# Kernel tuning notes

Hardware: AMD Instinct MI355X
Metric: run time of the kernel (lower is better)

## Reference

```python
import jax, jax.numpy as jnp
import numpy as np

B, S, D = 2, 2048, 2048
NH, NKV = 16, 4
HD = D // NH          # 128
Q_DIM = NH * HD       # 2048
KV_DIM = NKV * HD     # 512
N_REP = NH // NKV     # 4


def setup_inputs() -> dict:
    key = jax.random.key(0)
    k1, k2, k3, k4 = jax.random.split(key, 4)
    x = jax.random.normal(k1, (B, S, D), dtype=jnp.float32)
    freqs_cis = jax.random.normal(k2, (S, HD), dtype=jnp.float32)
    Wqkv = jax.random.normal(k3, (Q_DIM + 2 * KV_DIM, D), dtype=jnp.float32) * (D ** -0.5)
    Wo = jax.random.normal(k4, (D, Q_DIM), dtype=jnp.float32) * (Q_DIM ** -0.5)
    return {"x": x, "freqs_cis": freqs_cis, "Wqkv": Wqkv, "Wo": Wo}


def _apply_rope(xq, xk, freqs_cis):
    # xq: [B,S,NH,HD], xk: [B,S,NKV,HD], freqs_cis: [S,HD] viewed as [S,1,HD//2,2]
    f = freqs_cis.reshape(S, 1, HD // 2, 2)
    f0, f1 = f[..., 0], f[..., 1]  # broadcast over batch & heads

    def rot(t):
        shp = t.shape
        tp = t.reshape(*shp[:-1], HD // 2, 2)
        t0, t1 = tp[..., 0], tp[..., 1]
        # row1 = <x, (f0,f1)>;  row0 = <x, (f1,-f0)>  (matches torch flip+negate)
        row1 = t0 * f0 + t1 * f1
        row0 = t0 * f1 - t1 * f0
        return jnp.stack([row0, row1], axis=-1).reshape(shp)

    return rot(xq), rot(xk)


def reference(x, freqs_cis, Wqkv, Wo):
    # Fused QKV projection (exact path: all RLA sketch dims = 0)
    xqkv = jnp.einsum('bsd,od->bso', x, Wqkv)
    xq = xqkv[..., :Q_DIM].reshape(B, S, NH, HD)
    xk = xqkv[..., Q_DIM:Q_DIM + KV_DIM].reshape(B, S, NKV, HD)
    xv = xqkv[..., Q_DIM + KV_DIM:].reshape(B, S, NKV, HD)

    xq, xk = _apply_rope(xq, xk, freqs_cis)

    # [B,H,S,HD]
    xq = xq.transpose(0, 2, 1, 3)
    xk = xk.transpose(0, 2, 1, 3)
    xv = xv.transpose(0, 2, 1, 3)

    # GQA: repeat kv heads n_rep times
    xk = jnp.repeat(xk, N_REP, axis=1)
    xv = jnp.repeat(xv, N_REP, axis=1)

    scale = 1.0 / jnp.sqrt(jnp.asarray(HD, dtype=xq.dtype))
    scores = jnp.einsum('bhqd,bhkd->bhqk', xq, xk) * scale
    causal = jnp.tril(jnp.ones((S, S), dtype=bool))
    scores = jnp.where(causal, scores, jnp.finfo(scores.dtype).min)
    probs = jax.nn.softmax(scores, axis=-1)
    out = jnp.einsum('bhqk,bhkd->bhqd', probs, xv)  # [B,H,S,HD]

    out = out.transpose(0, 2, 1, 3).reshape(B, S, Q_DIM)
    return jnp.einsum('bsq,dq->bsd', out, Wo)
```

## Files before the change

kernel.cpp:

```cpp
#include <hip/hip_runtime.h>
#include <hip/hip_bf16.h>
#include <cstdint>
#include <cstddef>

#define B_ 2
#define S_ 2048
#define NH_ 16
#define NKV_ 4
#define HD_ 128
#define QDIM_ 2048
#define KVDIM_ 512
#define QKV_ 3072

typedef __attribute__((ext_vector_type(8))) short short8;
typedef __attribute__((ext_vector_type(4))) short bhalf4;
typedef __attribute__((ext_vector_type(4))) float float4v;

__device__ __forceinline__ float bf2f(short u) {
  union { unsigned int i; float f; } v;
  v.i = ((unsigned int)(unsigned short)u) << 16;
  return v.f;
}
__device__ __forceinline__ short f2bf(float f) {
  union { float f; unsigned int i; } v; v.f = f;
  unsigned int x = v.i;
  x += 0x7fffu + ((x >> 16) & 1u);
  return (short)(x >> 16);
}

#if __has_builtin(__builtin_amdgcn_exp2f)
__device__ __forceinline__ float exp2fast(float x) { return __builtin_amdgcn_exp2f(x); }
#else
__device__ __forceinline__ float exp2fast(float x) { return exp2f(x); }
#endif

__device__ __forceinline__ unsigned int cvt_pk_bf16(float a, float b) {
  unsigned int r;
  asm("v_cvt_pk_bf16_f32 %0, %1, %2" : "=v"(r) : "v"(a), "v"(b));
  return r;
}

__device__ __forceinline__ void async_copy16(void* lds, const void* g) {
  __builtin_amdgcn_global_load_lds(
      (const __attribute__((address_space(1))) void*)g,
      (__attribute__((address_space(3))) void*)lds, 16, 0, 0);
}

__global__ void f32_to_bf16(const float* __restrict__ src, short* __restrict__ dst,
                            int n8) {
  int id = blockIdx.x * 256 + threadIdx.x;
  if (id >= n8) return;
  const float* f = src + (size_t)id * 8;
  float4v a = *(const float4v*)(f);
  float4v b = *(const float4v*)(f + 4);
  short8 r;
#pragma unroll
  for (int e = 0; e < 4; ++e) { r[e] = f2bf(a[e]); r[4 + e] = f2bf(b[e]); }
  *(short8*)(dst + (size_t)id * 8) = r;
}

template <int N, int K, bool CF32>
__global__ __launch_bounds__(256)
void gemm_nt_bf16(const short* __restrict__ A, const short* __restrict__ Bm,
                  void* __restrict__ Cp) {
  __shared__ __align__(16) short sA[128 * 32];
  __shared__ __align__(16) short sB[128 * 32];
  const int tid = threadIdx.x;
  const int m0 = blockIdx.y * 128, n0 = blockIdx.x * 128;
  const int wave = tid >> 6, lane = tid & 63;
  const int wm = (wave & 1) << 6, wn = (wave >> 1) << 6;
  const int lm = lane & 15, kg = lane >> 4;

  float4v acc[4][4];
#pragma unroll
  for (int i = 0; i < 4; ++i)
#pragma unroll
    for (int j = 0; j < 4; ++j)
      acc[i][j] = (float4v){0.f, 0.f, 0.f, 0.f};

  const int r0 = tid >> 2, c0 = tid & 3;
  const short* gA0 = A + (size_t)(m0 + r0) * K + c0 * 8;
  const short* gA1 = gA0 + (size_t)64 * K;
  const short* gB0 = Bm + (size_t)(n0 + r0) * K + c0 * 8;
  const short* gB1 = gB0 + (size_t)64 * K;
  short* lA0 = sA + tid * 8;
  short* lA1 = sA + 2048 + tid * 8;
  short* lB0 = sB + tid * 8;
  short* lB1 = sB + 2048 + tid * 8;

  for (int k0 = 0; k0 < K; k0 += 32) {
    async_copy16(lA0, gA0 + k0);
    async_copy16(lA1, gA1 + k0);
    async_copy16(lB0, gB0 + k0);
    async_copy16(lB1, gB1 + k0);
    __syncthreads();

    short8 a[4], b[4];
#pragma unroll
    for (int i = 0; i < 4; ++i)
      a[i] = *(const short8*)(sA + (wm + i * 16 + lm) * 32 + kg * 8);
#pragma unroll
    for (int j = 0; j < 4; ++j)
      b[j] = *(const short8*)(sB + (wn + j * 16 + lm) * 32 + kg * 8);
#pragma unroll
    for (int i = 0; i < 4; ++i)
#pragma unroll
      for (int j = 0; j < 4; ++j)
        acc[i][j] = __builtin_amdgcn_mfma_f32_16x16x32_bf16(a[i], b[j], acc[i][j], 0, 0, 0);
    __syncthreads();
  }

#pragma unroll
  for (int i = 0; i < 4; ++i) {
    const int rb = m0 + wm + i * 16 + kg * 4;
#pragma unroll
    for (int j = 0; j < 4; ++j) {
      const int cc = n0 + wn + j * 16 + lm;
#pragma unroll
      for (int r = 0; r < 4; ++r) {
        if constexpr (CF32)
          ((float*)Cp)[(size_t)(rb + r) * N + cc] = acc[i][j][r];
        else
          ((short*)Cp)[(size_t)(rb + r) * N + cc] = f2bf(acc[i][j][r]);
      }
    }
  }
}

__global__ void rope_split(const short* __restrict__ xqkv, const float* __restrict__ freqs,
                           short* __restrict__ Qr, short* __restrict__ Kr,
                           short* __restrict__ Vv) {
  const int id = blockIdx.x * 256 + threadIdx.x;
  const int i = id / (QKV_ / 8);
  const int c8 = id % (QKV_ / 8);
  const int col = c8 * 8;
  const int b = i >> 11, s = i & (S_ - 1);
  short8 xv = *(const short8*)(xqkv + (size_t)i * QKV_ + col);
  if (col < QDIM_ + KVDIM_) {
    int d;
    short* dst;
    float sc;
    if (col < QDIM_) {
      int hh = col >> 7; d = col & 127;
      dst = Qr + ((size_t)(b * NH_ + hh) * S_ + s) * HD_ + d;
      sc = 0.12751744543795287f;
    } else {
      int cc = col - QDIM_;
      int hh = cc >> 7; d = cc & 127;
      dst = Kr + ((size_t)(b * NKV_ + hh) * S_ + s) * HD_ + d;
      sc = 1.0f;
    }
    const float* fp = freqs + (size_t)s * HD_ + d;
    float4v fa = *(const float4v*)(fp);
    float4v fb = *(const float4v*)(fp + 4);
    float ff[8] = {fa[0], fa[1], fa[2], fa[3], fb[0], fb[1], fb[2], fb[3]};
    short8 ov;
#pragma unroll
    for (int pp = 0; pp < 4; ++pp) {
      float t0 = bf2f(xv[2 * pp]), t1 = bf2f(xv[2 * pp + 1]);
      float f0 = ff[2 * pp], f1 = ff[2 * pp + 1];
      ov[2 * pp]     = f2bf((t0 * f1 - t1 * f0) * sc);
      ov[2 * pp + 1] = f2bf((t0 * f0 + t1 * f1) * sc);
    }
    *(short8*)dst = ov;
  } else {
    int cc = col - QDIM_ - KVDIM_;
    int hh = cc >> 7, d = cc & 127;
    *(short8*)(Vv + ((size_t)(b * NKV_ + hh) * S_ + s) * HD_ + d) = xv;
  }
}

__global__ void transpose_v(const short* __restrict__ Vv, short* __restrict__ Vt) {
  __shared__ short t[64][72];
  const int s0 = blockIdx.x * 64, d0 = blockIdx.y * 64;
  const short* src = Vv + (size_t)blockIdx.z * S_ * HD_;
  short* dst = Vt + (size_t)blockIdx.z * S_ * HD_;
  const int tid = threadIdx.x;
#pragma unroll
  for (int c = 0; c < 2; ++c) {
    int ch = tid + 256 * c;
    int row = ch >> 3, kc = ch & 7;
    *(short8*)(&t[row][kc * 8]) =
        *(const short8*)(src + (size_t)(s0 + row) * HD_ + d0 + kc * 8);
  }
  __syncthreads();
#pragma unroll
  for (int c = 0; c < 2; ++c) {
    int ch = tid + 256 * c;
    int drow = ch >> 3, sc = ch & 7;
    short8 w;
#pragma unroll
    for (int j = 0; j < 8; ++j) w[j] = t[sc * 8 + j][drow];
    *(short8*)(dst + (size_t)(d0 + drow) * S_ + s0 + sc * 8) = w;
  }
}

#define TK 64

__global__ __launch_bounds__(256, 4)
void attn_causal(const short* __restrict__ Q, const short* __restrict__ K,
                 const short* __restrict__ Vt, short* __restrict__ O) {
  const int bh = blockIdx.x;
  const int qt = 31 - (int)blockIdx.y;
  const int b = bh >> 4, h = bh & 15;
  const int kvh = h >> 2;
  const int tid = threadIdx.x, wave = tid >> 6, lane = tid & 63;
  const int lm = lane & 15, kg = lane >> 4;

  __shared__ __align__(16) short sK[TK * HD_];
  __shared__ __align__(16) short sVt[HD_ * TK];

  const short* Qb = Q + (size_t)(b * NH_ + h) * S_ * HD_;
  const short* Kb = K + (size_t)(b * NKV_ + kvh) * S_ * HD_;
  const short* Vtb = Vt + (size_t)(b * NKV_ + kvh) * S_ * HD_;

  auto stageK = [&](int k0) {
#pragma unroll
    for (int c = 0; c < 4; ++c) {
      int ch = tid + 256 * c;
      int row = ch >> 4, kc = ch & 15;
      async_copy16(sK + ch * 8,
                   Kb + (size_t)(k0 + row) * HD_ + (kc ^ (row & 7)) * 8);
    }
  };
  auto stageV = [&](int k0) {
#pragma unroll
    for (int c = 0; c < 4; ++c) {
      int ch = tid + 256 * c;
      int row = ch >> 3, kc = ch & 7;
      async_copy16(sVt + ch * 8,
                   Vtb + (size_t)row * S_ + k0 + (kc ^ (row & 7)) * 8);
    }
  };

  const int qglob = qt * 64 + wave * 16 + lm;
  short8 qf[4];
#pragma unroll
  for (int kk = 0; kk < 4; ++kk)
    qf[kk] = *(const short8*)(Qb + (size_t)qglob * HD_ + kk * 32 + kg * 8);

  float mcur = -1e9f, lcur = 0.f;
  float4v o[8];
#pragma unroll
  for (int df = 0; df < 8; ++df) o[df] = (float4v){0.f, 0.f, 0.f, 0.f};

  stageK(0);
  const int nst = qt + 1;
  for (int s = 0; s < nst; ++s) {
    const int k0 = s * TK;
    const bool diag = (s == qt);

    __syncthreads();
    stageV(k0);

    float4v sfT[4];
#pragma unroll
    for (int mj = 0; mj < 4; ++mj) sfT[mj] = (float4v){0.f, 0.f, 0.f, 0.f};
#pragma unroll
    for (int kk = 0; kk < 4; ++kk) {
      int kd = kk * 4 + kg;
#pragma unroll
      for (int mj = 0; mj < 4; ++mj) {
        int row = mj * 16 + lm;
        short8 af = *(const short8*)(sK + row * HD_ + (kd ^ (row & 7)) * 8);
        sfT[mj] = __builtin_amdgcn_mfma_f32_16x16x32_bf16(af, qf[kk], sfT[mj], 0, 0, 0);
      }
    }

    if (diag) {
#pragma unroll
      for (int mj = 0; mj < 4; ++mj)
#pragma unroll
        for (int r = 0; r < 4; ++r) {
          int kcol = k0 + mj * 16 + kg * 4 + r;
          sfT[mj][r] = (kcol <= qglob) ? sfT[mj][r] : -3e38f;
        }
    }

    float mx = -3e38f;
#pragma unroll
    for (int mj = 0; mj < 4; ++mj)
#pragma unroll
      for (int r = 0; r < 4; ++r) mx = fmaxf(mx, sfT[mj][r]);
    mx = fmaxf(mx, __shfl_xor(mx, 16, 64));
    mx = fmaxf(mx, __shfl_xor(mx, 32, 64));
    const bool need = (mx > mcur + 4.f);
    const float mnew = fmaxf(mcur, mx);
    const float alpha = need ? exp2fast(mcur - mnew) : 1.f;
    const float m_use = need ? mnew : mcur;
    float rs = 0.f;
    bhalf4 pb[4];
#pragma unroll
    for (int t = 0; t < 4; ++t) {
      float e0 = exp2fast(sfT[t][0] - m_use);
      float e1 = exp2fast(sfT[t][1] - m_use);
      float e2 = exp2fast(sfT[t][2] - m_use);
      float e3 = exp2fast(sfT[t][3] - m_use);
      rs += (e0 + e1) + (e2 + e3);
      union { unsigned int u[2]; bhalf4 v; } pk;
      pk.u[0] = cvt_pk_bf16(e0, e1);
      pk.u[1] = cvt_pk_bf16(e2, e3);
      pb[t] = pk.v;
    }
    rs += __shfl_xor(rs, 16, 64);
    rs += __shfl_xor(rs, 32, 64);
    mcur = m_use;
    lcur = lcur * alpha + rs;

    __syncthreads();
    if (s + 1 < nst) stageK(k0 + TK);

    if (__any(need)) {
#pragma unroll
      for (int df = 0; df < 8; ++df)
#pragma unroll
        for (int r = 0; r < 4; ++r) o[df][r] *= alpha;
    }

#pragma unroll
    for (int t = 0; t < 4; ++t) {
      int kc = t * 2 + (kg >> 1);
#pragma unroll
      for (int df = 0; df < 8; ++df) {
        int row = df * 16 + lm;
        bhalf4 va = *(const bhalf4*)(sVt + row * TK + (kc ^ (row & 7)) * 8 +
                                     (kg & 1) * 4);
        o[df] = __builtin_amdgcn_mfma_f32_16x16x16bf16_1k(va, pb[t], o[df], 0, 0, 0);
      }
    }
  }

  const float inv = 1.f / lcur;
  const size_t rowoff = (size_t)(b * S_ + qglob) * QDIM_ + h * HD_ + kg * 4;
#pragma unroll
  for (int df = 0; df < 8; ++df) {
    bhalf4 w;
    w[0] = f2bf(o[df][0] * inv);
    w[1] = f2bf(o[df][1] * inv);
    w[2] = f2bf(o[df][2] * inv);
    w[3] = f2bf(o[df][3] * inv);
    *(bhalf4*)(O + rowoff + df * 16) = w;
  }
}

extern "C" void kernel_launch(void* const* d_in, const int* in_sizes, int n_in,
                              void* d_out, int out_size, void* d_ws, size_t ws_size,
                              hipStream_t stream) {
  const float* x     = (const float*)d_in[0];
  const float* freqs = (const float*)d_in[1];
  const float* Wqkv  = (const float*)d_in[2];
  const float* Wo    = (const float*)d_in[3];
  float* out = (float*)d_out;

  short* ws     = (short*)d_ws;
  short* xb     = ws;
  short* Wob    = ws;
  short* Wqkvb  = ws + (size_t)4096 * 2048;
  short* xqkv   = Wqkvb + (size_t)QKV_ * 2048;
  short* attn   = xqkv;
  short* Qr     = xqkv + (size_t)4096 * QKV_;
  short* Kr     = Qr + (size_t)B_ * NH_ * S_ * HD_;
  short* Vv     = Kr + (size_t)B_ * NKV_ * S_ * HD_;
  short* Vtg    = Vv + (size_t)B_ * NKV_ * S_ * HD_;

  f32_to_bf16<<<(4096 * 2048 / 8) / 256, 256, 0, stream>>>(x, xb, 4096 * 2048 / 8);
  f32_to_bf16<<<(QKV_ * 2048 / 8) / 256, 256, 0, stream>>>(Wqkv, Wqkvb, QKV_ * 2048 / 8);
  gemm_nt_bf16<QKV_, 2048, false>
      <<<dim3(QKV_ / 128, 4096 / 128), 256, 0, stream>>>(xb, Wqkvb, xqkv);
  f32_to_bf16<<<(2048 * 2048 / 8) / 256, 256, 0, stream>>>(Wo, Wob, 2048 * 2048 / 8);
  rope_split<<<(B_ * S_ * QKV_ / 8) / 256, 256, 0, stream>>>(xqkv, freqs, Qr, Kr, Vv);
  transpose_v<<<dim3(S_ / 64, HD_ / 64, B_ * NKV_), 256, 0, stream>>>(Vv, Vtg);
  attn_causal<<<dim3(32, 32), 256, 0, stream>>>(Qr, Kr, Vtg, attn);
  gemm_nt_bf16<2048, 2048, true>
      <<<dim3(2048 / 128, 4096 / 128), 256, 0, stream>>>(attn, Wob, out);
}
```

Before: 318.8 us.

## Prefetch next K/V tile into registers and raise MFMA priority in attention

Replaces the async global-to-LDS copies of K and V with register prefetch of the next tile issued at the start of each iteration. The registers are written to LDS after the PV MFMAs, fenced by manual s_barrier and waitcnt. s_setprio is raised around both MFMA blocks so the matrix work is favoured over other waves. The aim is to hide global load latency behind the current tile's compute and cut the number of barriers, at the cost of 64 extra VGPRs, which may lower occupancy under launch_bounds(256,4).

```diff
diff --git a/kernel.cpp b/kernel.cpp
--- a/kernel.cpp
+++ b/kernel.cpp
@@ -214,24 +214,8 @@
   const short* Kb = K + (size_t)(b * NKV_ + kvh) * S_ * HD_;
   const short* Vtb = Vt + (size_t)(b * NKV_ + kvh) * S_ * HD_;
 
-  auto stageK = [&](int k0) {
-#pragma unroll
-    for (int c = 0; c < 4; ++c) {
-      int ch = tid + 256 * c;
-      int row = ch >> 4, kc = ch & 15;
-      async_copy16(sK + ch * 8,
-                   Kb + (size_t)(k0 + row) * HD_ + (kc ^ (row & 7)) * 8);
-    }
-  };
-  auto stageV = [&](int k0) {
-#pragma unroll
-    for (int c = 0; c < 4; ++c) {
-      int ch = tid + 256 * c;
-      int row = ch >> 3, kc = ch & 7;
-      async_copy16(sVt + ch * 8,
-                   Vtb + (size_t)row * S_ + k0 + (kc ^ (row & 7)) * 8);
-    }
-  };
+  const int rK = tid >> 4, cK = tid & 15;
+  const int rV = tid >> 3, cV = tid & 7;
 
   const int qglob = qt * 64 + wave * 16 + lm;
   short8 qf[4];
@@ -244,18 +228,46 @@
 #pragma unroll
   for (int df = 0; df < 8; ++df) o[df] = (float4v){0.f, 0.f, 0.f, 0.f};
 
-  stageK(0);
+  {
+    short8 kr[4], vr[4];
+#pragma unroll
+    for (int c = 0; c < 4; ++c) {
+      const int rowK = rK + 16 * c;
+      kr[c] = *(const short8*)(Kb + (size_t)rowK * HD_ + (cK ^ (rowK & 7)) * 8);
+      const int rowV = rV + 32 * c;
+      vr[c] = *(const short8*)(Vtb + (size_t)rowV * S_ + (cV ^ (rowV & 7)) * 8);
+    }
+#pragma unroll
+    for (int c = 0; c < 4; ++c) {
+      *(short8*)(sK + (tid + 256 * c) * 8) = kr[c];
+      *(short8*)(sVt + (tid + 256 * c) * 8) = vr[c];
+    }
+    __syncthreads();
+  }
+
   const int nst = qt + 1;
   for (int s = 0; s < nst; ++s) {
     const int k0 = s * TK;
     const bool diag = (s == qt);
-
-    __syncthreads();
-    stageV(k0);
+    const bool haveNext = (s + 1 < nst);
+
+    short8 kr[4], vr[4];
+    if (haveNext) {
+      const int k0n = k0 + TK;
+#pragma unroll
+      for (int c = 0; c < 4; ++c) {
+        const int rowK = rK + 16 * c;
+        kr[c] = *(const short8*)(Kb + (size_t)(k0n + rowK) * HD_ + (cK ^ (rowK & 7)) * 8);
+        const int rowV = rV + 32 * c;
+        vr[c] = *(const short8*)(Vtb + (size_t)rowV * S_ + k0n + (cV ^ (rowV & 7)) * 8);
+      }
+      asm volatile("" ::: "memory");
+    }
 
     float4v sfT[4];
 #pragma unroll
     for (int mj = 0; mj < 4; ++mj) sfT[mj] = (float4v){0.f, 0.f, 0.f, 0.f};
+    __builtin_amdgcn_s_setprio(1);
 #pragma unroll
     for (int kk = 0; kk < 4; ++kk) {
       int kd = kk * 4 + kg;
@@ -266,6 +278,7 @@
         sfT[mj] = __builtin_amdgcn_mfma_f32_16x16x32_bf16(af, qf[kk], sfT[mj], 0, 0, 0);
       }
     }
+    __builtin_amdgcn_s_setprio(0);
 
     if (diag) {
 #pragma unroll
@@ -307,9 +320,6 @@
     mcur = m_use;
     lcur = lcur * alpha + rs;
 
-    __syncthreads();
-    if (s + 1 < nst) stageK(k0 + TK);
-
     if (__any(need)) {
 #pragma unroll
       for (int df = 0; df < 8; ++df)
@@ -317,6 +327,7 @@
         for (int r = 0; r < 4; ++r) o[df][r] *= alpha;
     }
 
+    __builtin_amdgcn_s_setprio(1);
 #pragma unroll
     for (int t = 0; t < 4; ++t) {
       int kc = t * 2 + (kg >> 1);
@@ -327,6 +338,18 @@
                                      (kg & 1) * 4);
         o[df] = __builtin_amdgcn_mfma_f32_16x16x16bf16_1k(va, pb[t], o[df], 0, 0, 0);
       }
+    }
+    __builtin_amdgcn_s_setprio(0);
+
+    if (haveNext) {
+      asm volatile("s_barrier" ::: "memory");
+#pragma unroll
+      for (int c = 0; c < 4; ++c) {
+        *(short8*)(sK + (tid + 256 * c) * 8) = kr[c];
+        *(short8*)(sVt + (tid + 256 * c) * 8) = vr[c];
+      }
+      asm volatile("s_waitcnt lgkmcnt(0)" ::: "memory");
+      asm volatile("s_barrier" ::: "memory");
     }
   }
 
```

Measured after the change: 343.5 us. 1.08x slower.

## Double attention KV tile to 128, raise MFMA wave priority, merge input conversions

Applied to the files above, without the earlier changes.

The causal attention kernel now stages 128 keys per iteration instead of 64. This halves the loop trip count and the number of barriers and online-softmax rescales per query tile, and the causal mask moves to the last tile. LDS use doubles to 64KB and occupancy drops to 2 blocks per CU, which is the main risk. The MFMA sections are wrapped in s_setprio to favour matrix issue. The x and Wqkv fp32-to-bf16 conversions are merged into one launch to save launch overhead.

```diff
diff --git a/kernel.cpp b/kernel.cpp
--- a/kernel.cpp
+++ b/kernel.cpp
@@ -46,17 +46,32 @@
       (__attribute__((address_space(3))) void*)lds, 16, 0, 0);
 }
 
+__device__ __forceinline__ void cvt8(const float* f, short* d) {
+  float4v a = *(const float4v*)(f);
+  float4v b = *(const float4v*)(f + 4);
+  short8 r;
+#pragma unroll
+  for (int e = 0; e < 4; ++e) { r[e] = f2bf(a[e]); r[4 + e] = f2bf(b[e]); }
+  *(short8*)d = r;
+}
+
 __global__ void f32_to_bf16(const float* __restrict__ src, short* __restrict__ dst,
                             int n8) {
   int id = blockIdx.x * 256 + threadIdx.x;
   if (id >= n8) return;
-  const float* f = src + (size_t)id * 8;
-  float4v a = *(const float4v*)(f);
-  float4v b = *(const float4v*)(f + 4);
-  short8 r;
-#pragma unroll
-  for (int e = 0; e < 4; ++e) { r[e] = f2bf(a[e]); r[4 + e] = f2bf(b[e]); }
-  *(short8*)(dst + (size_t)id * 8) = r;
+  cvt8(src + (size_t)id * 8, dst + (size_t)id * 8);
+}
+
+__global__ void f32_to_bf16_2(const float* __restrict__ s0, short* __restrict__ d0,
+                              int n0_8, const float* __restrict__ s1,
+                              short* __restrict__ d1) {
+  int id = blockIdx.x * 256 + threadIdx.x;
+  if (id < n0_8) {
+    cvt8(s0 + (size_t)id * 8, d0 + (size_t)id * 8);
+  } else {
+    int j = id - n0_8;
+    cvt8(s1 + (size_t)j * 8, d1 + (size_t)j * 8);
+  }
 }
 
 template <int N, int K, bool CF32>
@@ -195,9 +210,9 @@
   }
 }
 
-#define TK 64
-
-__global__ __launch_bounds__(256, 4)
+#define TK 128
+
+__global__ __launch_bounds__(256, 2)
 void attn_causal(const short* __restrict__ Q, const short* __restrict__ K,
                  const short* __restrict__ Vt, short* __restrict__ O) {
   const int bh = blockIdx.x;
@@ -216,7 +231,7 @@
 
   auto stageK = [&](int k0) {
 #pragma unroll
-    for (int c = 0; c < 4; ++c) {
+    for (int c = 0; c < 8; ++c) {
       int ch = tid + 256 * c;
       int row = ch >> 4, kc = ch & 15;
       async_copy16(sK + ch * 8,
@@ -225,9 +240,9 @@
   };
   auto stageV = [&](int k0) {
 #pragma unroll
-    for (int c = 0; c < 4; ++c) {
+    for (int c = 0; c < 8; ++c) {
       int ch = tid + 256 * c;
-      int row = ch >> 3, kc = ch & 7;
+      int row = ch >> 4, kc = ch & 15;
       async_copy16(sVt + ch * 8,
                    Vtb + (size_t)row * S_ + k0 + (kc ^ (row & 7)) * 8);
     }
@@ -245,31 +260,33 @@
   for (int df = 0; df < 8; ++df) o[df] = (float4v){0.f, 0.f, 0.f, 0.f};
 
   stageK(0);
-  const int nst = qt + 1;
+  const int nst = (qt + 2) >> 1;
   for (int s = 0; s < nst; ++s) {
     const int k0 = s * TK;
-    const bool diag = (s == qt);
+    const bool last = (s == nst - 1);
 
     __syncthreads();
     stageV(k0);
 
-    float4v sfT[4];
-#pragma unroll
-    for (int mj = 0; mj < 4; ++mj) sfT[mj] = (float4v){0.f, 0.f, 0.f, 0.f};
+    float4v sfT[8];
+#pragma unroll
+    for (int mj = 0; mj < 8; ++mj) sfT[mj] = (float4v){0.f, 0.f, 0.f, 0.f};
+    __builtin_amdgcn_s_setprio(1);
 #pragma unroll
     for (int kk = 0; kk < 4; ++kk) {
       int kd = kk * 4 + kg;
 #pragma unroll
-      for (int mj = 0; mj < 4; ++mj) {
+      for (int mj = 0; mj < 8; ++mj) {
         int row = mj * 16 + lm;
         short8 af = *(const short8*)(sK + row * HD_ + (kd ^ (row & 7)) * 8);
         sfT[mj] = __builtin_amdgcn_mfma_f32_16x16x32_bf16(af, qf[kk], sfT[mj], 0, 0, 0);
       }
     }
-
-    if (diag) {
-#pragma unroll
-      for (int mj = 0; mj < 4; ++mj)
+    __builtin_amdgcn_s_setprio(0);
+
+    if (last) {
+#pragma unroll
+      for (int mj = 0; mj < 8; ++mj)
 #pragma unroll
         for (int r = 0; r < 4; ++r) {
           int kcol = k0 + mj * 16 + kg * 4 + r;
@@ -279,7 +296,7 @@
 
     float mx = -3e38f;
 #pragma unroll
-    for (int mj = 0; mj < 4; ++mj)
+    for (int mj = 0; mj < 8; ++mj)
 #pragma unroll
       for (int r = 0; r < 4; ++r) mx = fmaxf(mx, sfT[mj][r]);
     mx = fmaxf(mx, __shfl_xor(mx, 16, 64));
@@ -289,9 +306,9 @@
     const float alpha = need ? exp2fast(mcur - mnew) : 1.f;
     const float m_use = need ? mnew : mcur;
     float rs = 0.f;
-    bhalf4 pb[4];
-#pragma unroll
-    for (int t = 0; t < 4; ++t) {
+    bhalf4 pb[8];
+#pragma unroll
+    for (int t = 0; t < 8; ++t) {
       float e0 = exp2fast(sfT[t][0] - m_use);
       float e1 = exp2fast(sfT[t][1] - m_use);
       float e2 = exp2fast(sfT[t][2] - m_use);
@@ -308,7 +325,7 @@
     lcur = lcur * alpha + rs;
 
     __syncthreads();
-    if (s + 1 < nst) stageK(k0 + TK);
+    if (!last) stageK(k0 + TK);
 
     if (__any(need)) {
 #pragma unroll
@@ -317,8 +334,9 @@
         for (int r = 0; r < 4; ++r) o[df][r] *= alpha;
     }
 
-#pragma unroll
-    for (int t = 0; t < 4; ++t) {
+    __builtin_amdgcn_s_setprio(1);
+#pragma unroll
+    for (int t = 0; t < 8; ++t) {
       int kc = t * 2 + (kg >> 1);
 #pragma unroll
       for (int df = 0; df < 8; ++df) {
@@ -328,6 +346,7 @@
         o[df] = __builtin_amdgcn_mfma_f32_16x16x16bf16_1k(va, pb[t], o[df], 0, 0, 0);
       }
     }
+    __builtin_amdgcn_s_setprio(0);
   }
 
   const float inv = 1.f / lcur;
@@ -363,8 +382,8 @@
   short* Vv     = Kr + (size_t)B_ * NKV_ * S_ * HD_;
   short* Vtg    = Vv + (size_t)B_ * NKV_ * S_ * HD_;
 
-  f32_to_bf16<<<(4096 * 2048 / 8) / 256, 256, 0, stream>>>(x, xb, 4096 * 2048 / 8);
-  f32_to_bf16<<<(QKV_ * 2048 / 8) / 256, 256, 0, stream>>>(Wqkv, Wqkvb, QKV_ * 2048 / 8);
+  f32_to_bf16_2<<<(4096 * 2048 / 8 + QKV_ * 2048 / 8) / 256, 256, 0, stream>>>(
+      x, xb, 4096 * 2048 / 8, Wqkv, Wqkvb);
   gemm_nt_bf16<QKV_, 2048, false>
       <<<dim3(QKV_ / 128, 4096 / 128), 256, 0, stream>>>(xb, Wqkvb, xqkv);
   f32_to_bf16<<<(2048 * 2048 / 8) / 256, 256, 0, stream>>>(Wo, Wob, 2048 * 2048 / 8);
```

Result: faster. 309.6 us (-2.9%).
